# Kernel optimization log

Hardware: AMD Instinct MI355X
Metric: run time of the kernel (lower is better)

The kernel has to match this reference:

```python
import jax, jax.numpy as jnp
import numpy as np

LANE_WEIGHT = 1.0   # _LANE_LOSS_WEIGHT
TEMP = 0.1          # args.score_temp

B, L, K, T = 256, 16, 64, 50
NL, NT = B * L, B * L * K


def _seg_ids(starts, n):
    # contiguous segments covering [0, n): segment id = (# starts <= i) - 1
    return (jnp.cumsum(jnp.zeros((n,), jnp.int32).at[starts].add(1)) - 1).astype(jnp.int32)


def _seg_log_softmax(x, seg, nseg):
    m = jax.ops.segment_max(x, seg, num_segments=nseg)
    z = x - m[seg]
    lse = jnp.log(jax.ops.segment_sum(jnp.exp(z), seg, num_segments=nseg))
    return z - lse[seg]


def _seg_softmax(x, seg, nseg):
    m = jax.ops.segment_max(x, seg, num_segments=nseg)
    e = jnp.exp(x - m[seg])
    s = jax.ops.segment_sum(e, seg, num_segments=nseg)
    return e / s[seg]


def setup_inputs() -> dict:
    key = jax.random.key(0)
    k1, k2, k3, k4, k5 = jax.random.split(key, 5)
    lane_scores = jax.random.normal(k1, (NL,), jnp.float32)
    traj_scores = jax.random.normal(k2, (NT, 1), jnp.float32)
    pred_candidates = jax.random.normal(k3, (NT, T, 2), jnp.float32)
    pred_gt = jax.random.normal(k4, (B, T, 2), jnp.float32)
    scales = jnp.ones((B,), jnp.float32)
    # ragged segment boundaries (here uniform, but reference only uses starts)
    cls_start_end_idx = jnp.stack([jnp.arange(B, dtype=jnp.int32) * L,
                                   jnp.arange(B, dtype=jnp.int32) * L + L], axis=1)
    trajs_start_end_idx = jnp.stack([jnp.arange(NL, dtype=jnp.int32) * K,
                                     jnp.arange(NL, dtype=jnp.int32) * K + K], axis=1)
    cls_oracle = jax.random.bernoulli(k5, 0.3, (NL,))
    # guarantee >= 1 oracle lane per sample (original divides by len(traj_loss))
    cls_oracle = cls_oracle.at[jnp.arange(B) * L].set(True)
    return {
        "lane_scores": lane_scores,
        "traj_scores": traj_scores,
        "pred_candidates": pred_candidates,
        "pred_gt": pred_gt,
        "scales": scales,
        "cls_oracle": cls_oracle,
        "cls_start_end_idx": cls_start_end_idx,
        "trajs_start_end_idx": trajs_start_end_idx,
    }


def reference(lane_scores, traj_scores, pred_candidates, pred_gt, scales,
              cls_oracle, cls_start_end_idx, trajs_start_end_idx):
    nl, nt = lane_scores.shape[0], traj_scores.shape[0]
    b = cls_start_end_idx.shape[0]
    lane_sample = _seg_ids(cls_start_end_idx[:, 0], nl)   # [NL] -> sample id
    traj_lane = _seg_ids(trajs_start_end_idx[:, 0], nt)   # [NT] -> lane id
    traj_sample = lane_sample[traj_lane]                  # [NT] -> sample id

    # ---- lane-level cross entropy per sample ----
    oracle_f = cls_oracle.astype(lane_scores.dtype)
    oracle_per_sample = jax.ops.segment_sum(oracle_f, lane_sample, num_segments=b)
    lane_target = oracle_f / oracle_per_sample[lane_sample]
    lane_logp = _seg_log_softmax(lane_scores, lane_sample, b)
    lane_loss = jax.ops.segment_sum(-lane_target * lane_logp, lane_sample,
                                    num_segments=b) * LANE_WEIGHT  # [B]

    # ---- trajectory-level cross entropy per oracle lane ----
    # ScoreEvaluator.scoring_trajs: ADE distance to GT, scale-normalized, negated
    diff = pred_candidates - pred_gt[traj_sample]          # [NT, T, 2]
    ade = jnp.mean(jnp.sqrt(jnp.sum(diff * diff, axis=-1) + 1e-12), axis=-1)
    scores = -ade / scales[traj_sample]                    # [NT]

    target = _seg_softmax(scores / TEMP, traj_lane, nl)    # softmax(scores/temp)
    out_logp = _seg_log_softmax(traj_scores[:, 0], traj_lane, nl)
    ce_per_lane = jax.ops.segment_sum(-target * out_logp, traj_lane,
                                      num_segments=nl)     # [NL]
    # only oracle lanes contribute; average over oracle-lane count per sample
    traj_loss = jax.ops.segment_sum(ce_per_lane * oracle_f, lane_sample,
                                    num_segments=b) / oracle_per_sample  # [B]

    return jnp.mean(lane_loss + traj_loss)
```

## Files before the change

kernel.cpp:

```cpp
#include <hip/hip_runtime.h>
#include <math.h>


#define LANE_WEIGHT 1.0f
#define TEMP_INV    10.0f

#define TT     50
#define FPT    25
#define NWAVES 4

typedef float v4f __attribute__((ext_vector_type(4)));

typedef __attribute__((address_space(1))) const unsigned int gu32;
typedef __attribute__((address_space(3))) unsigned int       lu32;

__device__ __forceinline__ void stage16(const float* g, v4f* l)
{
    __builtin_amdgcn_global_load_lds((gu32*)g, (lu32*)l, 16, 0, 0);
}

__global__ __launch_bounds__(256) void dual_classify_fast(
    const float* __restrict__ pred_candidates,
    const float* __restrict__ pred_gt,
    const float* __restrict__ traj_scores,
    const float* __restrict__ scales,
    const float* __restrict__ lane_scores,
    const int*   __restrict__ cls_oracle,
    const int*   __restrict__ cls_se,
    const int*   __restrict__ trajs_se,
    float*       __restrict__ out,
    int B)
{
    __shared__ v4f   buf[NWAVES][64 * FPT];
    __shared__ v4f   s_gt[FPT];
    __shared__ float s_ce[64];

    const int sample = blockIdx.x;
    const int wid    = threadIdx.x >> 6;
    const int lid    = threadIdx.x & 63;

    const int cs = cls_se[2 * sample];
    const int nl = cls_se[2 * sample + 1] - cs;

    if (threadIdx.x < FPT)
        s_gt[threadIdx.x] =
            ((const v4f*)(pred_gt + (size_t)sample * (2 * TT)))[threadIdx.x];
    const float inv_scale = 1.0f / scales[sample];
    __syncthreads();

    for (int li = wid; li < nl; li += NWAVES) {
        const int lane = cs + li;
        const int t0   = trajs_se[2 * lane];
        const int Kl   = trajs_se[2 * lane + 1] - t0;
        const int NF   = Kl * FPT;

        const float* gbase  = pred_candidates + (size_t)t0 * (2 * TT);
        const int    ncalls = (NF + 63) >> 6;
        for (int r = 0; r < ncalls; ++r) {
            const int idx = (r << 6) + lid;
            if (idx < NF)
                stage16(gbase + (size_t)idx * 4, &buf[wid][r << 6]);
        }
        asm volatile("s_waitcnt vmcnt(0)" ::: "memory");

        const bool valid = (lid < Kl);
        float sum = 0.0f;
        {
            const v4f* tp = &buf[wid][lid * FPT];
            #pragma unroll 5
            for (int j = 0; j < FPT; ++j) {
                v4f c = tp[j];
                v4f g = s_gt[j];
                float dx0 = c.x - g.x, dy0 = c.y - g.y;
                float dx1 = c.z - g.z, dy1 = c.w - g.w;
                sum += sqrtf(dx0 * dx0 + dy0 * dy0 + 1e-12f)
                     + sqrtf(dx1 * dx1 + dy1 * dy1 + 1e-12f);
            }
        }

        float sc = valid ? (-(sum / (float)TT) * inv_scale * TEMP_INV)
                         : -INFINITY;
        float m = sc;
        for (int off = 32; off; off >>= 1) m = fmaxf(m, __shfl_xor(m, off));
        float e = valid ? expf(sc - m) : 0.0f;
        float Z = e;
        for (int off = 32; off; off >>= 1) Z += __shfl_xor(Z, off);
        float target = e / Z;

        const int traj = t0 + (valid ? lid : (Kl > 0 ? Kl - 1 : 0));
        float tsc = valid ? traj_scores[traj] : -INFINITY;
        float m2 = tsc;
        for (int off = 32; off; off >>= 1) m2 = fmaxf(m2, __shfl_xor(m2, off));
        float e2 = valid ? expf(tsc - m2) : 0.0f;
        float Z2 = e2;
        for (int off = 32; off; off >>= 1) Z2 += __shfl_xor(Z2, off);
        float logp = (tsc - m2) - logf(Z2);

        float ce = valid ? (-target * logp) : 0.0f;
        for (int off = 32; off; off >>= 1) ce += __shfl_xor(ce, off);
        if (lid == 0) s_ce[li] = ce;
    }
    __syncthreads();

    if (wid == 0) {
        const bool v = (lid < nl);
        const int  l = cs + (v ? lid : 0);

        float sc = v ? lane_scores[l] : -INFINITY;
        float m = sc;
        for (int off = 32; off; off >>= 1) m = fmaxf(m, __shfl_xor(m, off));
        float e = v ? expf(sc - m) : 0.0f;
        float Z = e;
        for (int off = 32; off; off >>= 1) Z += __shfl_xor(Z, off);
        const float lse = m + logf(Z);

        const bool o = v && (cls_oracle[l] != 0);
        float cnt = o ? 1.0f : 0.0f;
        float ll  = o ? -(sc - lse) : 0.0f;
        float tl  = o ? s_ce[lid]   : 0.0f;
        for (int off = 32; off; off >>= 1) {
            cnt += __shfl_xor(cnt, off);
            ll  += __shfl_xor(ll,  off);
            tl  += __shfl_xor(tl,  off);
        }
        if (lid == 0) {
            const float sample_loss = (ll * LANE_WEIGHT + tl) / cnt;
            atomicAdd(out, sample_loss / (float)B);
        }
    }
}

__global__ __launch_bounds__(1024) void dual_classify_sample(
    const float* __restrict__ pred_candidates,
    const float* __restrict__ pred_gt,
    const float* __restrict__ traj_scores,
    const float* __restrict__ scales,
    const float* __restrict__ lane_scores,
    const int*   __restrict__ cls_oracle,
    const int*   __restrict__ cls_se,
    const int*   __restrict__ trajs_se,
    float*       __restrict__ out,
    int B, int T)
{
    const int sample = blockIdx.x;
    const int wid    = threadIdx.x >> 6;
    const int lid    = threadIdx.x & 63;
    const int nwaves = blockDim.x >> 6;

    const int cs   = cls_se[2 * sample];
    const int cend = cls_se[2 * sample + 1];
    const int nl   = cend - cs;

    __shared__ float s_ce[64];

    const int nf4 = (T * 2) / 4;
    const v4f* __restrict__ gp =
        (const v4f*)(pred_gt + (size_t)sample * (T * 2));
    const float inv_scale = 1.0f / scales[sample];

    for (int li = wid; li < nl; li += nwaves) {
        const int lane = cs + li;
        const int t0 = trajs_se[2 * lane];
        const int Kl = trajs_se[2 * lane + 1] - t0;

        const bool valid = (lid < Kl);
        const int  traj  = t0 + (valid ? lid : (Kl > 0 ? Kl - 1 : 0));
        const v4f* __restrict__ tp =
            (const v4f*)(pred_candidates + (size_t)traj * (T * 2));

        float sum = 0.0f;
        #pragma unroll 5
        for (int r = 0; r < nf4; ++r) {
            v4f c = tp[r];
            v4f g = gp[r];
            float dx0 = c.x - g.x, dy0 = c.y - g.y;
            float dx1 = c.z - g.z, dy1 = c.w - g.w;
            sum += sqrtf(dx0 * dx0 + dy0 * dy0 + 1e-12f)
                 + sqrtf(dx1 * dx1 + dy1 * dy1 + 1e-12f);
        }
        if ((T & 1) != 0) {
            const float2* tp2 = (const float2*)tp;
            const float2* gp2 = (const float2*)gp;
            float2 c = tp2[2 * nf4], g = gp2[2 * nf4];
            float dx = c.x - g.x, dy = c.y - g.y;
            sum += sqrtf(dx * dx + dy * dy + 1e-12f);
        }

        float sc = valid ? (-(sum / (float)T) * inv_scale * TEMP_INV)
                         : -INFINITY;
        float m = sc;
        for (int off = 32; off; off >>= 1) m = fmaxf(m, __shfl_xor(m, off));
        float e = valid ? expf(sc - m) : 0.0f;
        float Z = e;
        for (int off = 32; off; off >>= 1) Z += __shfl_xor(Z, off);
        float target = e / Z;

        float tsc = valid ? traj_scores[traj] : -INFINITY;
        float m2 = tsc;
        for (int off = 32; off; off >>= 1) m2 = fmaxf(m2, __shfl_xor(m2, off));
        float e2 = valid ? expf(tsc - m2) : 0.0f;
        float Z2 = e2;
        for (int off = 32; off; off >>= 1) Z2 += __shfl_xor(Z2, off);
        float logp = (tsc - m2) - logf(Z2);

        float ce = valid ? (-target * logp) : 0.0f;
        for (int off = 32; off; off >>= 1) ce += __shfl_xor(ce, off);
        if (lid == 0) s_ce[li] = ce;
    }
    __syncthreads();

    if (wid == 0) {
        const bool v = (lid < nl);
        const int  l = cs + (v ? lid : 0);

        float sc = v ? lane_scores[l] : -INFINITY;
        float m = sc;
        for (int off = 32; off; off >>= 1) m = fmaxf(m, __shfl_xor(m, off));
        float e = v ? expf(sc - m) : 0.0f;
        float Z = e;
        for (int off = 32; off; off >>= 1) Z += __shfl_xor(Z, off);
        const float lse = m + logf(Z);

        const bool o = v && (cls_oracle[l] != 0);
        float cnt = o ? 1.0f : 0.0f;
        float ll  = o ? -(sc - lse) : 0.0f;
        float tl  = o ? s_ce[lid]   : 0.0f;
        for (int off = 32; off; off >>= 1) {
            cnt += __shfl_xor(cnt, off);
            ll  += __shfl_xor(ll,  off);
            tl  += __shfl_xor(tl,  off);
        }
        if (lid == 0) {
            const float sample_loss = (ll * LANE_WEIGHT + tl) / cnt;
            atomicAdd(out, sample_loss / (float)B);
        }
    }
}

extern "C" void kernel_launch(void* const* d_in, const int* in_sizes, int n_in,
                              void* d_out, int out_size, void* d_ws, size_t ws_size,
                              hipStream_t stream)
{
    const float* lane_scores     = (const float*)d_in[0];
    const float* traj_scores     = (const float*)d_in[1];
    const float* pred_candidates = (const float*)d_in[2];
    const float* pred_gt         = (const float*)d_in[3];
    const float* scales          = (const float*)d_in[4];
    const int*   cls_oracle      = (const int*)d_in[5];
    const int*   cls_se          = (const int*)d_in[6];
    const int*   trajs_se        = (const int*)d_in[7];

    const int NT = in_sizes[1];
    const int B  = in_sizes[6] / 2;
    const int T  = in_sizes[2] / (NT * 2);

    float* out = (float*)d_out;

    if (T == TT) {
        dual_classify_fast<<<B, NWAVES * 64, 0, stream>>>(
            pred_candidates, pred_gt, traj_scores, scales, lane_scores,
            cls_oracle, cls_se, trajs_se, out, B);
    } else {
        dual_classify_sample<<<B, 1024, 0, stream>>>(
            pred_candidates, pred_gt, traj_scores, scales, lane_scores,
            cls_oracle, cls_se, trajs_se, out, B, T);
    }
}
```

Measured before the change: 180.0 us.

## Load trajectories directly into registers instead of staging through LDS, use 8 waves

Replaces the global_load_lds staging of each lane's trajectory block into shared memory with direct per-thread vector loads of that thread's 25 float4s into registers. It also doubles the waves per block to 8 and raises the launch bounds to 512. Each thread now reads a strided, uncoalesced 400-byte row, which relies on cache lines being shared across neighbouring threads. In exchange the large LDS buffer and the full vmcnt wait are gone, and more waves are resident to hide latency.

```diff
diff --git a/kernel.cpp b/kernel.cpp
--- a/kernel.cpp
+++ b/kernel.cpp
@@ -7,19 +7,11 @@
 
 #define TT     50
 #define FPT    25
-#define NWAVES 4
+#define NWAVES 8
 
 typedef float v4f __attribute__((ext_vector_type(4)));
 
-typedef __attribute__((address_space(1))) const unsigned int gu32;
-typedef __attribute__((address_space(3))) unsigned int       lu32;
-
-__device__ __forceinline__ void stage16(const float* g, v4f* l)
-{
-    __builtin_amdgcn_global_load_lds((gu32*)g, (lu32*)l, 16, 0, 0);
-}
-
-__global__ __launch_bounds__(256) void dual_classify_fast(
+__global__ __launch_bounds__(512) void dual_classify_fast(
     const float* __restrict__ pred_candidates,
     const float* __restrict__ pred_gt,
     const float* __restrict__ traj_scores,
@@ -31,7 +23,6 @@
     float*       __restrict__ out,
     int B)
 {
-    __shared__ v4f   buf[NWAVES][64 * FPT];
     __shared__ v4f   s_gt[FPT];
     __shared__ float s_ce[64];
 
@@ -52,30 +43,25 @@
         const int lane = cs + li;
         const int t0   = trajs_se[2 * lane];
         const int Kl   = trajs_se[2 * lane + 1] - t0;
-        const int NF   = Kl * FPT;
-
-        const float* gbase  = pred_candidates + (size_t)t0 * (2 * TT);
-        const int    ncalls = (NF + 63) >> 6;
-        for (int r = 0; r < ncalls; ++r) {
-            const int idx = (r << 6) + lid;
-            if (idx < NF)
-                stage16(gbase + (size_t)idx * 4, &buf[wid][r << 6]);
-        }
-        asm volatile("s_waitcnt vmcnt(0)" ::: "memory");
 
         const bool valid = (lid < Kl);
+        const int  traj  = t0 + (valid ? lid : (Kl > 0 ? Kl - 1 : 0));
+        const v4f* __restrict__ tp =
+            (const v4f*)(pred_candidates + (size_t)traj * (2 * TT));
+
+        v4f c[FPT];
+        #pragma unroll
+        for (int j = 0; j < FPT; ++j) c[j] = tp[j];
+        __builtin_amdgcn_sched_barrier(0);
+
         float sum = 0.0f;
-        {
-            const v4f* tp = &buf[wid][lid * FPT];
-            #pragma unroll 5
-            for (int j = 0; j < FPT; ++j) {
-                v4f c = tp[j];
-                v4f g = s_gt[j];
-                float dx0 = c.x - g.x, dy0 = c.y - g.y;
-                float dx1 = c.z - g.z, dy1 = c.w - g.w;
-                sum += sqrtf(dx0 * dx0 + dy0 * dy0 + 1e-12f)
-                     + sqrtf(dx1 * dx1 + dy1 * dy1 + 1e-12f);
-            }
+        #pragma unroll
+        for (int j = 0; j < FPT; ++j) {
+            v4f g = s_gt[j];
+            float dx0 = c[j].x - g.x, dy0 = c[j].y - g.y;
+            float dx1 = c[j].z - g.z, dy1 = c[j].w - g.w;
+            sum += sqrtf(dx0 * dx0 + dy0 * dy0 + 1e-12f)
+                 + sqrtf(dx1 * dx1 + dy1 * dy1 + 1e-12f);
         }
 
         float sc = valid ? (-(sum / (float)TT) * inv_scale * TEMP_INV)
@@ -87,7 +73,6 @@
         for (int off = 32; off; off >>= 1) Z += __shfl_xor(Z, off);
         float target = e / Z;
 
-        const int traj = t0 + (valid ? lid : (Kl > 0 ? Kl - 1 : 0));
         float tsc = valid ? traj_scores[traj] : -INFINITY;
         float m2 = tsc;
         for (int off = 32; off; off >>= 1) m2 = fmaxf(m2, __shfl_xor(m2, off));
```

Result: no change. 179.4 us (-0.3%).
